# Kernel tuning notes

Measured on AMD Instinct MI355X. Metric: run time of the kernel, lower is better.

## Reference

```python
import jax, jax.numpy as jnp
import numpy as np

D = 768
H = 12
DH = D // H
EPS = 1e-5

def _ln(x, g, b):
    m = jnp.mean(x, axis=-1, keepdims=True)
    v = jnp.mean(jnp.square(x - m), axis=-1, keepdims=True)
    return (x - m) * jax.lax.rsqrt(v + EPS) * g + b

def _gelu_new(x):
    c = jnp.float32(0.7978845608028654)  # sqrt(2/pi)
    return 0.5 * x * (1.0 + jnp.tanh(c * (x + 0.044715 * x * x * x)))

def setup_inputs() -> dict:
    key = jax.random.key(0)
    ks = jax.random.split(key, 12)
    s = lambda fan: 1.0 / np.sqrt(fan)
    return {
        "x": jax.random.normal(ks[0], (2, 1024, D), jnp.float32),
        "context_seq": jax.random.normal(ks[1], (2, 256, D), jnp.float32),
        "sos_h": jnp.zeros((D,), jnp.float32),
        "ln1_g": jnp.ones((D,), jnp.float32),
        "ln1_b": jnp.zeros((D,), jnp.float32),
        "W_attn": jax.random.normal(ks[2], (D, 3 * D), jnp.float32) * s(D),
        "b_attn": jnp.zeros((3 * D,), jnp.float32),
        "W_ref": jax.random.normal(ks[3], (D, 2 * D), jnp.float32) * s(D),
        "b_ref": jnp.zeros((2 * D,), jnp.float32),
        "W_proj": jax.random.normal(ks[4], (D, D), jnp.float32) * s(D),
        "b_proj": jnp.zeros((D,), jnp.float32),
        "ln2_g": jnp.ones((D,), jnp.float32),
        "ln2_b": jnp.zeros((D,), jnp.float32),
        "W_fc": jax.random.normal(ks[5], (D, 4 * D), jnp.float32) * s(D),
        "b_fc": jnp.zeros((4 * D,), jnp.float32),
        "W_mproj": jax.random.normal(ks[6], (4 * D, D), jnp.float32) * s(4 * D),
        "b_mproj": jnp.zeros((D,), jnp.float32),
    }

def _split_heads(t):  # [B,T,D] -> [B,H,T,dh]
    B, T, _ = t.shape
    return t.reshape(B, T, H, DH).transpose(0, 2, 1, 3)

def reference(x, context_seq, sos_h, ln1_g, ln1_b, W_attn, b_attn, W_ref, b_ref,
              W_proj, b_proj, ln2_g, ln2_b, W_fc, b_fc, W_mproj, b_mproj):
    B, S, _ = x.shape
    Sc = context_seq.shape[1]
    # prepend sos token (history_seq is None, history_seq_len = 0)
    sos = jnp.broadcast_to(sos_h.reshape(1, 1, D), (B, 1, D))
    h = jnp.concatenate([sos, x], axis=1)          # [B, S+1, D]
    hl = _ln(h, ln1_g, ln1_b)
    qkv = hl @ W_attn + b_attn
    q, k, v = jnp.split(qkv, 3, axis=-1)
    ckv = context_seq @ W_ref + b_ref
    kc, vc = jnp.split(ckv, 2, axis=-1)
    K = jnp.concatenate([kc, k], axis=1)            # [B, Sc+S+1, D]
    V = jnp.concatenate([vc, v], axis=1)
    qh, kh, vh = _split_heads(q), _split_heads(K), _split_heads(V)
    nd, ns = S + 1, Sc + S + 1
    w = jnp.einsum('bhqd,bhkd->bhqk', qh, kh) / jnp.float32(np.sqrt(DH))
    # causal bias window: query i attends to key j iff j <= i + Sc
    mask = jnp.arange(ns)[None, :] <= (jnp.arange(nd)[:, None] + Sc)
    w = jnp.where(mask[None, None], w, jnp.float32(-10000.0))
    w = jax.nn.softmax(w, axis=-1)
    a = jnp.einsum('bhqk,bhkd->bhqd', w, vh)        # [B,H,S+1,dh]
    a = a.transpose(0, 2, 1, 3).reshape(B, nd, D)
    a = a @ W_proj + b_proj
    h = h + a
    m = _gelu_new(_ln(h, ln2_g, ln2_b) @ W_fc + b_fc) @ W_mproj + b_mproj
    h = h + m
    return h[:, 1:, :]                               # drop sos position
```

## Files before the change

### kernel.cpp

```cpp
#include <hip/hip_runtime.h>
#include <math.h>

#define D0 768
#define NH 12
#define DHD 64
#define NB 2
#define SQ 1024
#define SCX 256
#define ND 1025
#define NS 1281
#define TT (NB*ND)
#define TP 2176
#define TC (NB*SCX)

typedef __attribute__((ext_vector_type(8))) short bf16x8;
typedef __attribute__((ext_vector_type(4))) float f32x4;

typedef const __attribute__((address_space(1))) unsigned int* gptr_t;
typedef __attribute__((address_space(3))) unsigned int* lptr_t;

__device__ __forceinline__ unsigned short f2bf(float f) {
    union { float f; unsigned u; } v; v.f = f;
    unsigned r = v.u + 0x7FFFu + ((v.u >> 16) & 1u);
    return (unsigned short)(r >> 16);
}

__device__ __forceinline__ float gelu_new(float x) {
    float x3 = x*x*x;
    float u = 0.7978845608028654f*(x + 0.044715f*x3);
    return 0.5f*x*(1.f + tanhf(u));
}

struct PrepArgs {
    const float* x; const float* sos; float* h;
    const float* ctx; unsigned short* ctxb;
    const float* W[5]; unsigned short* Wt[5];
    int K[5], N[5], nblk[5];
};

#define NBH 1538
#define NCVT 192

__global__ __launch_bounds__(256) void k_prep(PrepArgs a) {
    __shared__ float t[32][33];
    const int tid = threadIdx.x;
    int bid = blockIdx.x;
    if (bid < NBH) {
        int idx = bid*256 + tid;
        if (idx < TT*192) {
            int r = idx/192, c4 = idx%192;
            int b = r/ND, tt = r%ND;
            float4 v;
            if (tt == 0) v = ((const float4*)a.sos)[c4];
            else         v = ((const float4*)a.x)[(size_t)(b*SQ + tt - 1)*192 + c4];
            ((float4*)a.h)[(size_t)r*192 + c4] = v;
        }
        return;
    }
    bid -= NBH;
    if (bid < NCVT) {
        int i = bid*256 + tid;
        float4 p = ((const float4*)a.ctx)[i*2];
        float4 q = ((const float4*)a.ctx)[i*2+1];
        uint4 o;
        o.x = (unsigned)f2bf(p.x) | ((unsigned)f2bf(p.y) << 16);
        o.y = (unsigned)f2bf(p.z) | ((unsigned)f2bf(p.w) << 16);
        o.z = (unsigned)f2bf(q.x) | ((unsigned)f2bf(q.y) << 16);
        o.w = (unsigned)f2bf(q.z) | ((unsigned)f2bf(q.w) << 16);
        ((uint4*)a.ctxb)[i] = o;
        return;
    }
    bid -= NCVT;
    #pragma unroll
    for (int wi = 0; wi < 5; ++wi) {
        if (bid < a.nblk[wi]) {
            const float* W = a.W[wi];
            unsigned short* Wt = a.Wt[wi];
            const int K = a.K[wi], N = a.N[wi];
            const int nbx = N >> 5;
            const int n0 = (bid % nbx)*32, k0 = (bid / nbx)*32;
            const int r = tid >> 3, c4 = (tid & 7)*4;
            float4 v = *(const float4*)&W[(size_t)(k0+r)*N + n0 + c4];
            t[r][c4+0]=v.x; t[r][c4+1]=v.y; t[r][c4+2]=v.z; t[r][c4+3]=v.w;
            __syncthreads();
            ushort4 o;
            o.x = f2bf(t[c4+0][r]); o.y = f2bf(t[c4+1][r]);
            o.z = f2bf(t[c4+2][r]); o.w = f2bf(t[c4+3][r]);
            *(ushort4*)&Wt[(size_t)(n0+r)*K + k0 + c4] = o;
            return;
        }
        bid -= a.nblk[wi];
    }
}

__global__ __launch_bounds__(256) void k_ln(const float* __restrict__ in,
                                            const float* __restrict__ add,
                                            const float* __restrict__ g,
                                            const float* __restrict__ beta,
                                            unsigned short* __restrict__ out,
                                            float* __restrict__ resid,
                                            int nvalid) {
    int r = blockIdx.x;
    int tid = threadIdx.x;
    const size_t base = (size_t)r*D0;
    if (r >= nvalid) {
        out[base+tid] = 0; out[base+tid+256] = 0; out[base+tid+512] = 0;
        return;
    }
    float v0 = in[base+tid], v1 = in[base+tid+256], v2 = in[base+tid+512];
    if (add) {
        v0 += add[base+tid]; v1 += add[base+tid+256]; v2 += add[base+tid+512];
        resid[base+tid] = v0; resid[base+tid+256] = v1; resid[base+tid+512] = v2;
    }
    float s = v0+v1+v2;
    float ss = v0*v0 + v1*v1 + v2*v2;
    #pragma unroll
    for (int o = 32; o >= 1; o >>= 1) {
        s  += __shfl_down(s, o);
        ss += __shfl_down(ss, o);
    }
    __shared__ float red[8];
    __shared__ float mv[2];
    int w = tid >> 6;
    if ((tid & 63) == 0) { red[w] = s; red[4+w] = ss; }
    __syncthreads();
    if (tid == 0) {
        float S1 = red[0]+red[1]+red[2]+red[3];
        float S2 = red[4]+red[5]+red[6]+red[7];
        float mean = S1 * (1.f/D0);
        float var  = S2 * (1.f/D0) - mean*mean;
        mv[0] = mean; mv[1] = rsqrtf(var + 1e-5f);
    }
    __syncthreads();
    float mean = mv[0], rstd = mv[1];
    out[base+tid]     = f2bf((v0-mean)*rstd*g[tid]     + beta[tid]);
    out[base+tid+256] = f2bf((v1-mean)*rstd*g[tid+256] + beta[tid+256]);
    out[base+tid+512] = f2bf((v2-mean)*rstd*g[tid+512] + beta[tid+512]);
}

template<int GELU, int OUTBF>
__global__ __launch_bounds__(256) void k_gemm64(const unsigned short* __restrict__ A,
                                                const unsigned short* __restrict__ Bt,
                                                const float* __restrict__ bias,
                                                void* __restrict__ Cv,
                                                int M, int N, int K) {
    __shared__ unsigned short As[64*64];
    __shared__ unsigned short Bs[64*64];
    const int tid = threadIdx.x;
    const int w = tid >> 6;
    const int l = tid & 63;
    const int wm = w >> 1, wn = w & 1;
    const int m0 = blockIdx.y * 64, n0 = blockIdx.x * 64;

    f32x4 acc[2][2] = {};

    for (int k0 = 0; k0 < K; k0 += 64) {
        __syncthreads();
        #pragma unroll
        for (int i = 0; i < 2; ++i) {
            int s = i*256 + tid;
            int row = s >> 3;
            int ch  = (s & 7) ^ (row & 7);
            const unsigned short* ga = A  + (size_t)(m0 + row)*K + k0 + ch*8;
            const unsigned short* gb = Bt + (size_t)(n0 + row)*K + k0 + ch*8;
            lptr_t la = (lptr_t)(As + (i*256 + w*64)*8);
            lptr_t lb = (lptr_t)(Bs + (i*256 + w*64)*8);
            __builtin_amdgcn_global_load_lds((gptr_t)ga, la, 16, 0, 0);
            __builtin_amdgcn_global_load_lds((gptr_t)gb, lb, 16, 0, 0);
        }
        __syncthreads();
        #pragma unroll
        for (int kc = 0; kc < 2; ++kc) {
            const int kchunk = kc*4 + (l >> 4);
            bf16x8 a[2], b[2];
            #pragma unroll
            for (int mi = 0; mi < 2; ++mi) {
                int row = wm*32 + mi*16 + (l & 15);
                a[mi] = *(const bf16x8*)&As[row*64 + ((kchunk ^ (row & 7))*8)];
            }
            #pragma unroll
            for (int ni = 0; ni < 2; ++ni) {
                int row = wn*32 + ni*16 + (l & 15);
                b[ni] = *(const bf16x8*)&Bs[row*64 + ((kchunk ^ (row & 7))*8)];
            }
            #pragma unroll
            for (int mi = 0; mi < 2; ++mi)
                #pragma unroll
                for (int ni = 0; ni < 2; ++ni)
                    acc[mi][ni] = __builtin_amdgcn_mfma_f32_16x16x32_bf16(a[mi], b[ni], acc[mi][ni], 0, 0, 0);
        }
    }

    float* Cf = (float*)Cv;
    unsigned short* Cb = (unsigned short*)Cv;
    const int rbase = m0 + wm*32 + (l >> 4)*4;
    const int cbase = n0 + wn*32 + (l & 15);
    #pragma unroll
    for (int ni = 0; ni < 2; ++ni) {
        int col = cbase + ni*16;
        float bv = bias[col];
        #pragma unroll
        for (int mi = 0; mi < 2; ++mi) {
            #pragma unroll
            for (int r = 0; r < 4; ++r) {
                int row = rbase + mi*16 + r;
                float v = acc[mi][ni][r] + bv;
                if (GELU) v = gelu_new(v);
                if (OUTBF) Cb[(size_t)row*N + col] = f2bf(v);
                else       Cf[(size_t)row*N + col] = v;
            }
        }
    }
}

__global__ __launch_bounds__(256) void k_attn_mfma(const unsigned short* __restrict__ qkvb,
                                                   const unsigned short* __restrict__ ckvb,
                                                   unsigned short* __restrict__ attnob) {
    const int bh = blockIdx.y;
    const int b = bh / NH, hh = bh % NH;
    const int tid = threadIdx.x;
    const int w = tid >> 6;
    const int l = tid & 63;
    const int lg = l >> 4;
    const int ll = l & 15;

    const int q0 = blockIdx.x * 128;
    const int qw = q0 + w*32;

    __shared__ unsigned short Ks[64*64];
    __shared__ unsigned short Vt[64*64];
    __shared__ unsigned short Ps[4][32*64];

    bf16x8 qf[2][2];
    #pragma unroll
    for (int qt = 0; qt < 2; ++qt) {
        int q = qw + qt*16 + ll;
        int qc = min(q, ND-1);
        const unsigned short* qrow = qkvb + (size_t)(b*ND + qc)*2304 + hh*64;
        #pragma unroll
        for (int kc = 0; kc < 2; ++kc)
            qf[qt][kc] = *(const bf16x8*)(qrow + kc*32 + lg*8);
    }

    f32x4 o_acc[2][4] = {};
    float mrow[2][4], lrow[2][4];
    #pragma unroll
    for (int qt = 0; qt < 2; ++qt)
        #pragma unroll
        for (int i = 0; i < 4; ++i) { mrow[qt][i] = -1e30f; lrow[qt][i] = 0.f; }

    const int qmax_blk = min(q0 + 127, ND-1);
    const int ntiles = (qmax_blk + SCX)/64 + 1;
    const int qmax_wave = qw + 31;

    for (int kt = 0; kt < ntiles; ++kt) {
        __syncthreads();
        #pragma unroll
        for (int it = 0; it < 2; ++it) {
            int slot = w*128 + it*64 + l;
            int key  = slot >> 3;
            int ch   = (slot & 7) ^ (key & 7);
            int kg   = min(kt*64 + key, NS-1);
            const unsigned short* src;
            if (kg < SCX) src = ckvb + (size_t)(b*SCX + kg)*1536 + hh*64 + ch*8;
            else          src = qkvb + (size_t)(b*ND + kg - SCX)*2304 + 768 + hh*64 + ch*8;
            __builtin_amdgcn_global_load_lds((gptr_t)src, (lptr_t)(Ks + (size_t)(w*128 + it*64)*8), 16, 0, 0);
        }
        {
            int kp  = tid >> 3;
            int dch = tid & 7;
            int kv0 = kp*2;
            int kg0 = min(kt*64 + kv0,     NS-1);
            int kg1 = min(kt*64 + kv0 + 1, NS-1);
            const unsigned short* s0 = (kg0 < SCX)
                ? ckvb + (size_t)(b*SCX + kg0)*1536 + 768 + hh*64 + dch*8
                : qkvb + (size_t)(b*ND + kg0 - SCX)*2304 + 1536 + hh*64 + dch*8;
            const unsigned short* s1 = (kg1 < SCX)
                ? ckvb + (size_t)(b*SCX + kg1)*1536 + 768 + hh*64 + dch*8
                : qkvb + (size_t)(b*ND + kg1 - SCX)*2304 + 1536 + hh*64 + dch*8;
            union { uint4 u; unsigned short s[8]; } r0, r1;
            r0.u = *(const uint4*)s0;
            r1.u = *(const uint4*)s1;
            #pragma unroll
            for (int i = 0; i < 8; ++i) {
                int d = dch*8 + i;
                unsigned val = (unsigned)r0.s[i] | ((unsigned)r1.s[i] << 16);
                *(unsigned*)((char*)Vt + d*128 + (((kv0>>3) ^ (d&7))*16) + ((kv0&7)*2)) = val;
            }
        }
        __syncthreads();

        if (kt*64 > qmax_wave + SCX) continue;

        bf16x8 kf[4][2];
        #pragma unroll
        for (int c = 0; c < 4; ++c) {
            int key = c*16 + ll;
            #pragma unroll
            for (int kc = 0; kc < 2; ++kc)
                kf[c][kc] = *(const bf16x8*)((char*)Ks + key*128 + (((kc*4 + lg) ^ (key&7))*16));
        }
        f32x4 s_acc[2][4];
        #pragma unroll
        for (int qt = 0; qt < 2; ++qt)
            #pragma unroll
            for (int c = 0; c < 4; ++c) {
                f32x4 z = {0.f, 0.f, 0.f, 0.f};
                z = __builtin_amdgcn_mfma_f32_16x16x32_bf16(qf[qt][0], kf[c][0], z, 0, 0, 0);
                s_acc[qt][c] = __builtin_amdgcn_mfma_f32_16x16x32_bf16(qf[qt][1], kf[c][1], z, 0, 0, 0);
            }

        const int kbase = kt*64;
        if (kbase + 63 > qw + SCX) {
            #pragma unroll
            for (int qt = 0; qt < 2; ++qt)
                #pragma unroll
                for (int c = 0; c < 4; ++c) {
                    int key = kbase + c*16 + ll;
                    #pragma unroll
                    for (int i = 0; i < 4; ++i) {
                        int q = qw + qt*16 + lg*4 + i;
                        if (key > q + SCX) s_acc[qt][c][i] = -1e30f;
                    }
                }
        }

        #pragma unroll
        for (int qt = 0; qt < 2; ++qt) {
            float tmax[4];
            #pragma unroll
            for (int i = 0; i < 4; ++i) {
                float tm = fmaxf(fmaxf(s_acc[qt][0][i], s_acc[qt][1][i]),
                                 fmaxf(s_acc[qt][2][i], s_acc[qt][3][i]));
                #pragma unroll
                for (int o = 1; o < 16; o <<= 1) tm = fmaxf(tm, __shfl_xor(tm, o));
                tmax[i] = tm;
            }
            #pragma unroll
            for (int i = 0; i < 4; ++i) {
                float mnew = fmaxf(mrow[qt][i], tmax[i]*0.125f);
                float fs = __expf(mrow[qt][i] - mnew);
                mrow[qt][i] = mnew;
                lrow[qt][i] *= fs;
                #pragma unroll
                for (int dc = 0; dc < 4; ++dc) o_acc[qt][dc][i] *= fs;
            }
            float psum[4] = {0.f, 0.f, 0.f, 0.f};
            #pragma unroll
            for (int c = 0; c < 4; ++c) {
                int kv = c*16 + ll;
                #pragma unroll
                for (int i = 0; i < 4; ++i) {
                    float p = __expf(fmaf(s_acc[qt][c][i], 0.125f, -mrow[qt][i]));
                    psum[i] += p;
                    int q = qt*16 + lg*4 + i;
                    union { float f; unsigned u; } cv; cv.f = p;
                    *(unsigned short*)((char*)Ps[w] + q*128 + (((kv>>3) ^ (q&7))*16) + ((kv&7)*2))
                        = (unsigned short)((cv.u + 0x8000u) >> 16);
                }
            }
            #pragma unroll
            for (int i = 0; i < 4; ++i) {
                float s = psum[i];
                #pragma unroll
                for (int o = 1; o < 16; o <<= 1) s += __shfl_xor(s, o);
                lrow[qt][i] += s;
            }
        }

        #pragma unroll
        for (int kc = 0; kc < 2; ++kc) {
            bf16x8 pf[2], vf;
            #pragma unroll
            for (int qt = 0; qt < 2; ++qt) {
                int q = qt*16 + ll;
                pf[qt] = *(const bf16x8*)((char*)Ps[w] + q*128 + (((kc*4 + lg) ^ (q&7))*16));
            }
            #pragma unroll
            for (int dc = 0; dc < 4; ++dc) {
                int d = dc*16 + ll;
                vf = *(const bf16x8*)((char*)Vt + d*128 + (((kc*4 + lg) ^ (d&7))*16));
                #pragma unroll
                for (int qt = 0; qt < 2; ++qt)
                    o_acc[qt][dc] = __builtin_amdgcn_mfma_f32_16x16x32_bf16(pf[qt], vf, o_acc[qt][dc], 0, 0, 0);
            }
        }
    }

    #pragma unroll
    for (int qt = 0; qt < 2; ++qt) {
        #pragma unroll
        for (int i = 0; i < 4; ++i) {
            int q = qw + qt*16 + lg*4 + i;
            if (q >= ND) continue;
            float inv = 1.f / lrow[qt][i];
            unsigned short* orow = attnob + (size_t)(b*ND + q)*768 + hh*64;
            #pragma unroll
            for (int dc = 0; dc < 4; ++dc)
                orow[dc*16 + ll] = f2bf(o_acc[qt][dc][i] * inv);
        }
    }
}

__global__ void k_final(const float* __restrict__ h, const float* __restrict__ mp,
                        float* __restrict__ out) {
    int idx = blockIdx.x*blockDim.x + threadIdx.x;
    const int total = NB*SQ*192;
    if (idx >= total) return;
    int r = idx/192, c4 = idx%192;
    int b = r/SQ, t = r%SQ;
    size_t hr = (size_t)(b*ND + t + 1)*192 + c4;
    float4 hv = ((const float4*)h)[hr];
    float4 mv = ((const float4*)mp)[hr];
    ((float4*)out)[idx] = make_float4(hv.x+mv.x, hv.y+mv.y, hv.z+mv.z, hv.w+mv.w);
}

extern "C" void kernel_launch(void* const* d_in, const int* in_sizes, int n_in,
                              void* d_out, int out_size, void* d_ws, size_t ws_size,
                              hipStream_t stream) {
    const float* x     = (const float*)d_in[0];
    const float* ctx   = (const float*)d_in[1];
    const float* sos   = (const float*)d_in[2];
    const float* ln1g  = (const float*)d_in[3];
    const float* ln1b  = (const float*)d_in[4];
    const float* Wat   = (const float*)d_in[5];
    const float* bat   = (const float*)d_in[6];
    const float* Wref  = (const float*)d_in[7];
    const float* bref  = (const float*)d_in[8];
    const float* Wpj   = (const float*)d_in[9];
    const float* bpj   = (const float*)d_in[10];
    const float* ln2g  = (const float*)d_in[11];
    const float* ln2b  = (const float*)d_in[12];
    const float* Wfc   = (const float*)d_in[13];
    const float* bfc   = (const float*)d_in[14];
    const float* Wmp   = (const float*)d_in[15];
    const float* bmp   = (const float*)d_in[16];
    float* out = (float*)d_out;

    char* p = (char*)d_ws;
    float* h      = (float*)p;  p += (size_t)TP*768*4;
    float* aproj  = (float*)p;  p += (size_t)TP*768*4;
    unsigned short* qkvb   = (unsigned short*)p;  p += (size_t)TP*2304*2;
    unsigned short* ckvb   = (unsigned short*)p;  p += (size_t)TC*1536*2;
    unsigned short* hlb    = (unsigned short*)p;  p += (size_t)TP*768*2;
    unsigned short* attnob = (unsigned short*)p;  p += (size_t)TP*768*2;
    unsigned short* mfcb   = (unsigned short*)p;  p += (size_t)TP*3072*2;
    unsigned short* ctxb   = (unsigned short*)p;  p += (size_t)TC*768*2;
    unsigned short* WatT   = (unsigned short*)p;  p += (size_t)2304*768*2;
    unsigned short* WrefT  = (unsigned short*)p;  p += (size_t)1536*768*2;
    unsigned short* WpjT   = (unsigned short*)p;  p += (size_t)768*768*2;
    unsigned short* WfcT   = (unsigned short*)p;  p += (size_t)3072*768*2;
    unsigned short* WmpT   = (unsigned short*)p;  p += (size_t)768*3072*2;

    PrepArgs pa;
    pa.x = x; pa.sos = sos; pa.h = h; pa.ctx = ctx; pa.ctxb = ctxb;
    pa.W[0]=Wat;  pa.Wt[0]=WatT;  pa.K[0]=768;  pa.N[0]=2304; pa.nblk[0]=(2304/32)*(768/32);
    pa.W[1]=Wref; pa.Wt[1]=WrefT; pa.K[1]=768;  pa.N[1]=1536; pa.nblk[1]=(1536/32)*(768/32);
    pa.W[2]=Wpj;  pa.Wt[2]=WpjT;  pa.K[2]=768;  pa.N[2]=768;  pa.nblk[2]=(768/32)*(768/32);
    pa.W[3]=Wfc;  pa.Wt[3]=WfcT;  pa.K[3]=768;  pa.N[3]=3072; pa.nblk[3]=(3072/32)*(768/32);
    pa.W[4]=Wmp;  pa.Wt[4]=WmpT;  pa.K[4]=3072; pa.N[4]=768;  pa.nblk[4]=(768/32)*(3072/32);
    int nprep = NBH + NCVT + pa.nblk[0]+pa.nblk[1]+pa.nblk[2]+pa.nblk[3]+pa.nblk[4];

    k_prep<<<dim3(nprep), dim3(256), 0, stream>>>(pa);
    k_ln<<<dim3(TP), dim3(256), 0, stream>>>(h, nullptr, ln1g, ln1b, hlb, nullptr, TT);
    k_gemm64<0,1><<<dim3(2304/64, TP/64), dim3(256), 0, stream>>>(hlb, WatT, bat, qkvb, TP, 2304, 768);
    k_gemm64<0,1><<<dim3(1536/64, TC/64), dim3(256), 0, stream>>>(ctxb, WrefT, bref, ckvb, TC, 1536, 768);
    k_attn_mfma<<<dim3(9, NB*NH), dim3(256), 0, stream>>>(qkvb, ckvb, attnob);
    k_gemm64<0,0><<<dim3(768/64, TP/64), dim3(256), 0, stream>>>(attnob, WpjT, bpj, aproj, TP, 768, 768);
    k_ln<<<dim3(TP), dim3(256), 0, stream>>>(h, aproj, ln2g, ln2b, hlb, h, TT);
    k_gemm64<1,1><<<dim3(3072/64, TP/64), dim3(256), 0, stream>>>(hlb, WfcT, bfc, mfcb, TP, 3072, 768);
    k_gemm64<0,0><<<dim3(768/64, TP/64), dim3(256), 0, stream>>>(mfcb, WmpT, bmp, aproj, TP, 768, 3072);
    k_final<<<dim3((NB*SQ*192 + 255)/256), dim3(256), 0, stream>>>(h, aproj, out);
}
```

Before: 282.9 us.

## Fuse QKV and context-KV GEMMs; shrink attention query tiles and reverse block order

The two projection GEMMs (QKV over hidden states and KV over context) now run as one launch, with a linear block index split between the two problems. This removes one launch and fills the GPU with more concurrent blocks. The attention kernel now handles 64 queries per block (16 per wave), so it launches 17 query blocks per head instead of 9. Blocks are issued in reverse order so the longest causal rows start first, and launch_bounds asks for 2 blocks per SM. In exchange, each K/V tile loaded into LDS is reused across fewer queries, so global and LDS traffic per query goes up.

Measured after the change: 255.3 us. 1.11x faster.

```diff
diff --git a/kernel.cpp b/kernel.cpp
--- a/kernel.cpp
+++ b/kernel.cpp
@@ -139,18 +139,17 @@
 }
 
 template<int GELU, int OUTBF>
-__global__ __launch_bounds__(256) void k_gemm64(const unsigned short* __restrict__ A,
-                                                const unsigned short* __restrict__ Bt,
-                                                const float* __restrict__ bias,
-                                                void* __restrict__ Cv,
-                                                int M, int N, int K) {
-    __shared__ unsigned short As[64*64];
-    __shared__ unsigned short Bs[64*64];
+__device__ __forceinline__ void gemm64_body(unsigned short* As, unsigned short* Bs,
+                                            const unsigned short* __restrict__ A,
+                                            const unsigned short* __restrict__ Bt,
+                                            const float* __restrict__ bias,
+                                            void* __restrict__ Cv,
+                                            int N, int K, int bx, int by) {
     const int tid = threadIdx.x;
     const int w = tid >> 6;
     const int l = tid & 63;
     const int wm = w >> 1, wn = w & 1;
-    const int m0 = blockIdx.y * 64, n0 = blockIdx.x * 64;
+    const int m0 = by * 64, n0 = bx * 64;
 
     f32x4 acc[2][2] = {};
 
@@ -213,9 +212,39 @@
     }
 }
 
-__global__ __launch_bounds__(256) void k_attn_mfma(const unsigned short* __restrict__ qkvb,
-                                                   const unsigned short* __restrict__ ckvb,
-                                                   unsigned short* __restrict__ attnob) {
+template<int GELU, int OUTBF>
+__global__ __launch_bounds__(256) void k_gemm64(const unsigned short* __restrict__ A,
+                                                const unsigned short* __restrict__ Bt,
+                                                const float* __restrict__ bias,
+                                                void* __restrict__ Cv,
+                                                int N, int K) {
+    __shared__ unsigned short As[64*64];
+    __shared__ unsigned short Bs[64*64];
+    gemm64_body<GELU,OUTBF>(As, Bs, A, Bt, bias, Cv, N, K, blockIdx.x, blockIdx.y);
+}
+
+__global__ __launch_bounds__(256) void k_gemm_qkvckv(const unsigned short* __restrict__ hlb,
+                                                     const unsigned short* __restrict__ WatT,
+                                                     const float* __restrict__ bat,
+                                                     unsigned short* __restrict__ qkvb,
+                                                     const unsigned short* __restrict__ ctxb,
+                                                     const unsigned short* __restrict__ WrefT,
+                                                     const float* __restrict__ bref,
+                                                     unsigned short* __restrict__ ckvb) {
+    __shared__ unsigned short As[64*64];
+    __shared__ unsigned short Bs[64*64];
+    int bid = blockIdx.x;
+    if (bid < (2304/64)*(TP/64)) {
+        gemm64_body<0,1>(As, Bs, hlb, WatT, bat, qkvb, 2304, 768, bid % (2304/64), bid / (2304/64));
+    } else {
+        bid -= (2304/64)*(TP/64);
+        gemm64_body<0,1>(As, Bs, ctxb, WrefT, bref, ckvb, 1536, 768, bid % (1536/64), bid / (1536/64));
+    }
+}
+
+__global__ __launch_bounds__(256, 2) void k_attn_mfma(const unsigned short* __restrict__ qkvb,
+                                                      const unsigned short* __restrict__ ckvb,
+                                                      unsigned short* __restrict__ attnob) {
     const int bh = blockIdx.y;
     const int b = bh / NH, hh = bh % NH;
     const int tid = threadIdx.x;
@@ -224,52 +253,46 @@
     const int lg = l >> 4;
     const int ll = l & 15;
 
-    const int q0 = blockIdx.x * 128;
-    const int qw = q0 + w*32;
+    const int q0 = (16 - blockIdx.x) * 64;
+    const int qw = q0 + w*16;
 
     __shared__ unsigned short Ks[64*64];
     __shared__ unsigned short Vt[64*64];
-    __shared__ unsigned short Ps[4][32*64];
-
-    bf16x8 qf[2][2];
+    __shared__ unsigned short Ps[4][16*64];
+
+    bf16x8 qf[2];
+    {
+        int qc = min(qw + ll, ND-1);
+        const unsigned short* qrow = qkvb + (size_t)(b*ND + qc)*2304 + hh*64;
+        qf[0] = *(const bf16x8*)(qrow + lg*8);
+        qf[1] = *(const bf16x8*)(qrow + 32 + lg*8);
+    }
+
+    f32x4 o_acc[4] = {};
+    float mrow[4], lrow[4];
     #pragma unroll
-    for (int qt = 0; qt < 2; ++qt) {
-        int q = qw + qt*16 + ll;
-        int qc = min(q, ND-1);
-        const unsigned short* qrow = qkvb + (size_t)(b*ND + qc)*2304 + hh*64;
-        #pragma unroll
-        for (int kc = 0; kc < 2; ++kc)
-            qf[qt][kc] = *(const bf16x8*)(qrow + kc*32 + lg*8);
-    }
-
-    f32x4 o_acc[2][4] = {};
-    float mrow[2][4], lrow[2][4];
-    #pragma unroll
-    for (int qt = 0; qt < 2; ++qt)
-        #pragma unroll
-        for (int i = 0; i < 4; ++i) { mrow[qt][i] = -1e30f; lrow[qt][i] = 0.f; }
-
-    const int qmax_blk = min(q0 + 127, ND-1);
+    for (int i = 0; i < 4; ++i) { mrow[i] = -1e30f; lrow[i] = 0.f; }
+
+    const int qmax_blk = min(q0 + 63, ND-1);
     const int ntiles = (qmax_blk + SCX)/64 + 1;
-    const int qmax_wave = qw + 31;
+    const int klim_wave = qw + 15 + SCX;
 
     for (int kt = 0; kt < ntiles; ++kt) {
         __syncthreads();
         #pragma unroll
         for (int it = 0; it < 2; ++it) {
-            int slot = w*128 + it*64 + l;
+            int slot = it*256 + tid;
             int key  = slot >> 3;
             int ch   = (slot & 7) ^ (key & 7);
             int kg   = min(kt*64 + key, NS-1);
             const unsigned short* src;
             if (kg < SCX) src = ckvb + (size_t)(b*SCX + kg)*1536 + hh*64 + ch*8;
             else          src = qkvb + (size_t)(b*ND + kg - SCX)*2304 + 768 + hh*64 + ch*8;
-            __builtin_amdgcn_global_load_lds((gptr_t)src, (lptr_t)(Ks + (size_t)(w*128 + it*64)*8), 16, 0, 0);
+            __builtin_amdgcn_global_load_lds((gptr_t)src, (lptr_t)(Ks + (size_t)(it*256 + w*64)*8), 16, 0, 0);
         }
         {
-            int kp  = tid >> 3;
-            int dch = tid & 7;
-            int kv0 = kp*2;
+            int kv0 = (tid & 31)*2;
+            int dch = tid >> 5;
             int kg0 = min(kt*64 + kv0,     NS-1);
             int kg1 = min(kt*64 + kv0 + 1, NS-1);
             const unsigned short* s0 = (kg0 < SCX)
@@ -290,7 +313,7 @@
         }
         __syncthreads();
 
-        if (kt*64 > qmax_wave + SCX) continue;
+        if (kt*64 > klim_wave) continue;
 
         bf16x8 kf[4][2];
         #pragma unroll
@@ -300,105 +323,89 @@
             for (int kc = 0; kc < 2; ++kc)
                 kf[c][kc] = *(const bf16x8*)((char*)Ks + key*128 + (((kc*4 + lg) ^ (key&7))*16));
         }
-        f32x4 s_acc[2][4];
-        #pragma unroll
-        for (int qt = 0; qt < 2; ++qt)
-            #pragma unroll
-            for (int c = 0; c < 4; ++c) {
-                f32x4 z = {0.f, 0.f, 0.f, 0.f};
-                z = __builtin_amdgcn_mfma_f32_16x16x32_bf16(qf[qt][0], kf[c][0], z, 0, 0, 0);
-                s_acc[qt][c] = __builtin_amdgcn_mfma_f32_16x16x32_bf16(qf[qt][1], kf[c][1], z, 0, 0, 0);
-            }
+        f32x4 s_acc[4];
+        #pragma unroll
+        for (int c = 0; c < 4; ++c) {
+            f32x4 z = {0.f, 0.f, 0.f, 0.f};
+            z = __builtin_amdgcn_mfma_f32_16x16x32_bf16(qf[0], kf[c][0], z, 0, 0, 0);
+            s_acc[c] = __builtin_amdgcn_mfma_f32_16x16x32_bf16(qf[1], kf[c][1], z, 0, 0, 0);
+        }
 
         const int kbase = kt*64;
         if (kbase + 63 > qw + SCX) {
             #pragma unroll
-            for (int qt = 0; qt < 2; ++qt)
-                #pragma unroll
-                for (int c = 0; c < 4; ++c) {
-                    int key = kbase + c*16 + ll;
-                    #pragma unroll
-                    for (int i = 0; i < 4; ++i) {
-                        int q = qw + qt*16 + lg*4 + i;
-                        if (key > q + SCX) s_acc[qt][c][i] = -1e30f;
-                    }
-                }
-        }
-
-        #pragma unroll
-        for (int qt = 0; qt < 2; ++qt) {
-            float tmax[4];
-            #pragma unroll
-            for (int i = 0; i < 4; ++i) {
-                float tm = fmaxf(fmaxf(s_acc[qt][0][i], s_acc[qt][1][i]),
-                                 fmaxf(s_acc[qt][2][i], s_acc[qt][3][i]));
-                #pragma unroll
-                for (int o = 1; o < 16; o <<= 1) tm = fmaxf(tm, __shfl_xor(tm, o));
-                tmax[i] = tm;
-            }
-            #pragma unroll
-            for (int i = 0; i < 4; ++i) {
-                float mnew = fmaxf(mrow[qt][i], tmax[i]*0.125f);
-                float fs = __expf(mrow[qt][i] - mnew);
-                mrow[qt][i] = mnew;
-                lrow[qt][i] *= fs;
-                #pragma unroll
-                for (int dc = 0; dc < 4; ++dc) o_acc[qt][dc][i] *= fs;
-            }
-            float psum[4] = {0.f, 0.f, 0.f, 0.f};
-            #pragma unroll
             for (int c = 0; c < 4; ++c) {
-                int kv = c*16 + ll;
+                int key = kbase + c*16 + ll;
                 #pragma unroll
                 for (int i = 0; i < 4; ++i) {
-                    float p = __expf(fmaf(s_acc[qt][c][i], 0.125f, -mrow[qt][i]));
-                    psum[i] += p;
-                    int q = qt*16 + lg*4 + i;
-                    union { float f; unsigned u; } cv; cv.f = p;
-                    *(unsigned short*)((char*)Ps[w] + q*128 + (((kv>>3) ^ (q&7))*16) + ((kv&7)*2))
-                        = (unsigned short)((cv.u + 0x8000u) >> 16);
+                    int q = qw + lg*4 + i;
+                    if (key > q + SCX) s_acc[c][i] = -1e30f;
                 }
             }
+        }
+
+        float tmax[4];
+        #pragma unroll
+        for (int i = 0; i < 4; ++i) {
+            float tm = fmaxf(fmaxf(s_acc[0][i], s_acc[1][i]),
+                             fmaxf(s_acc[2][i], s_acc[3][i]));
+            #pragma unroll
+            for (int o = 1; o < 16; o <<= 1) tm = fmaxf(tm, __shfl_xor(tm, o));
+            tmax[i] = tm;
+        }
+        #pragma unroll
+        for (int i = 0; i < 4; ++i) {
+            float mnew = fmaxf(mrow[i], tmax[i]*0.125f);
+            float fs = __expf(mrow[i] - mnew);
+            mrow[i] = mnew;
+            lrow[i] *= fs;
+            #pragma unroll
+            for (int dc = 0; dc < 4; ++dc) o_acc[dc][i] *= fs;
+        }
+        float psum[4] = {0.f, 0.f, 0.f, 0.f};
+        #pragma unroll
+        for (int c = 0; c < 4; ++c) {
+            int kv = c*16 + ll;
             #pragma unroll
             for (int i = 0; i < 4; ++i) {
-                float s = psum[i];
-                #pragma unroll
-                for (int o = 1; o < 16; o <<= 1) s += __shfl_xor(s, o);
-                lrow[qt][i] += s;
-            }
+                float p = __expf(fmaf(s_acc[c][i], 0.125f, -mrow[i]));
+                psum[i] += p;
+                int q = lg*4 + i;
+                union { float f; unsigned u; } cv; cv.f = p;
+                *(unsigned short*)((char*)Ps[w] + q*128 + (((kv>>3) ^ (q&7))*16) + ((kv&7)*2))
+                    = (unsigned short)((cv.u + 0x8000u) >> 16);
+            }
+        }
+        #pragma unroll
+        for (int i = 0; i < 4; ++i) {
+            float s = psum[i];
+            #pragma unroll
+            for (int o = 1; o < 16; o <<= 1) s += __shfl_xor(s, o);
+            lrow[i] += s;
         }
 
         #pragma unroll
         for (int kc = 0; kc < 2; ++kc) {
-            bf16x8 pf[2], vf;
-            #pragma unroll
-            for (int qt = 0; qt < 2; ++qt) {
-                int q = qt*16 + ll;
-                pf[qt] = *(const bf16x8*)((char*)Ps[w] + q*128 + (((kc*4 + lg) ^ (q&7))*16));
-            }
+            int q = ll;
+            bf16x8 pf = *(const bf16x8*)((char*)Ps[w] + q*128 + (((kc*4 + lg) ^ (q&7))*16));
             #pragma unroll
             for (int dc = 0; dc < 4; ++dc) {
                 int d = dc*16 + ll;
-                vf = *(const bf16x8*)((char*)Vt + d*128 + (((kc*4 + lg) ^ (d&7))*16));
-                #pragma unroll
-                for (int qt = 0; qt < 2; ++qt)
-                    o_acc[qt][dc] = __builtin_amdgcn_mfma_f32_16x16x32_bf16(pf[qt], vf, o_acc[qt][dc], 0, 0, 0);
+                bf16x8 vf = *(const bf16x8*)((char*)Vt + d*128 + (((kc*4 + lg) ^ (d&7))*16));
+                o_acc[dc] = __builtin_amdgcn_mfma_f32_16x16x32_bf16(pf, vf, o_acc[dc], 0, 0, 0);
             }
         }
     }
 
     #pragma unroll
-    for (int qt = 0; qt < 2; ++qt) {
-        #pragma unroll
-        for (int i = 0; i < 4; ++i) {
-            int q = qw + qt*16 + lg*4 + i;
-            if (q >= ND) continue;
-            float inv = 1.f / lrow[qt][i];
-            unsigned short* orow = attnob + (size_t)(b*ND + q)*768 + hh*64;
-            #pragma unroll
-            for (int dc = 0; dc < 4; ++dc)
-                orow[dc*16 + ll] = f2bf(o_acc[qt][dc][i] * inv);
-        }
+    for (int i = 0; i < 4; ++i) {
+        int q = qw + lg*4 + i;
+        if (q >= ND) continue;
+        float inv = 1.f / lrow[i];
+        unsigned short* orow = attnob + (size_t)(b*ND + q)*768 + hh*64;
+        #pragma unroll
+        for (int dc = 0; dc < 4; ++dc)
+            orow[dc*16 + ll] = f2bf(o_acc[dc][i] * inv);
     }
 }
 
@@ -463,12 +470,12 @@
 
     k_prep<<<dim3(nprep), dim3(256), 0, stream>>>(pa);
     k_ln<<<dim3(TP), dim3(256), 0, stream>>>(h, nullptr, ln1g, ln1b, hlb, nullptr, TT);
-    k_gemm64<0,1><<<dim3(2304/64, TP/64), dim3(256), 0, stream>>>(hlb, WatT, bat, qkvb, TP, 2304, 768);
-    k_gemm64<0,1><<<dim3(1536/64, TC/64), dim3(256), 0, stream>>>(ctxb, WrefT, bref, ckvb, TC, 1536, 768);
-    k_attn_mfma<<<dim3(9, NB*NH), dim3(256), 0, stream>>>(qkvb, ckvb, attnob);
-    k_gemm64<0,0><<<dim3(768/64, TP/64), dim3(256), 0, stream>>>(attnob, WpjT, bpj, aproj, TP, 768, 768);
+    k_gemm_qkvckv<<<dim3((2304/64)*(TP/64) + (1536/64)*(TC/64)), dim3(256), 0, stream>>>(
+        hlb, WatT, bat, qkvb, ctxb, WrefT, bref, ckvb);
+    k_attn_mfma<<<dim3(17, NB*NH), dim3(256), 0, stream>>>(qkvb, ckvb, attnob);
+    k_gemm64<0,0><<<dim3(768/64, TP/64), dim3(256), 0, stream>>>(attnob, WpjT, bpj, aproj, 768, 768);
     k_ln<<<dim3(TP), dim3(256), 0, stream>>>(h, aproj, ln2g, ln2b, hlb, h, TT);
-    k_gemm64<1,1><<<dim3(3072/64, TP/64), dim3(256), 0, stream>>>(hlb, WfcT, bfc, mfcb, TP, 3072, 768);
-    k_gemm64<0,0><<<dim3(768/64, TP/64), dim3(256), 0, stream>>>(mfcb, WmpT, bmp, aproj, TP, 768, 3072);
+    k_gemm64<1,1><<<dim3(3072/64, TP/64), dim3(256), 0, stream>>>(hlb, WfcT, bfc, mfcb, 3072, 768);
+    k_gemm64<0,0><<<dim3(768/64, TP/64), dim3(256), 0, stream>>>(mfcb, WmpT, bmp, aproj, 768, 3072);
     k_final<<<dim3((NB*SQ*192 + 255)/256), dim3(256), 0, stream>>>(h, aproj, out);
 }
```
